# Kernel optimization log

Hardware: AMD Instinct MI355X
Metric: run time of the kernel (lower is better)

## Reference

```python
import jax, jax.numpy as jnp
import numpy as np

D = 1024
H = 8
B, S = 4, 2048


def setup_inputs() -> dict:
    key = jax.random.key(0)
    ks = jax.random.split(key, 11)
    s = 0.02
    return {
        "Q": jax.random.normal(ks[0], (B, S, D), jnp.float32),
        "K": jax.random.normal(ks[1], (B, S, D), jnp.float32),
        "V": jax.random.normal(ks[2], (B, S, D), jnp.float32),
        "WQ": jax.random.normal(ks[3], (D, D), jnp.float32) * s,
        "bQ": jax.random.normal(ks[4], (D,), jnp.float32) * s,
        "WK": jax.random.normal(ks[5], (D, D), jnp.float32) * s,
        "bK": jax.random.normal(ks[6], (D,), jnp.float32) * s,
        "WV": jax.random.normal(ks[7], (D, D), jnp.float32) * s,
        "bV": jax.random.normal(ks[8], (D,), jnp.float32) * s,
        "Wl": jax.random.normal(ks[9], (D, D * H), jnp.float32) * s,
        "bl": jax.random.normal(ks[10], (D,), jnp.float32) * s,
    }


def reference(Q, K, V, WQ, bQ, WK, bK, WV, bV, Wl, bl):
    # SelfAttention (weights shared across all heads in the original module)
    q = Q @ WQ.T + bQ  # [B,S,D]
    k = K @ WK.T + bK
    v = V @ WV.T + bV
    scale = 1.0 / np.sqrt(D).astype(np.float32)
    scores = jnp.einsum('bqd,bkd->bqk', q, k) * scale  # [B,S,S]
    attn = jax.nn.softmax(scores, axis=-1)
    Z = jnp.einsum('bqk,bkd->bqd', attn, v)  # [B,S,D]
    # concat of H identical copies, then linear(D*H -> D)
    Zcat = jnp.tile(Z, (1, 1, H))  # [B,S,D*H]
    return Zcat @ Wl.T + bl
```

## Files before the change

kernel.cpp:

```cpp
#include <hip/hip_runtime.h>
#include <stdint.h>

#define DEV __device__ __forceinline__

typedef __attribute__((ext_vector_type(8))) unsigned short frag8;
typedef __attribute__((ext_vector_type(4))) float f32x4;
typedef __attribute__((ext_vector_type(8))) unsigned short ushort8;
typedef __attribute__((ext_vector_type(4))) unsigned short ushort4v;

DEV unsigned short f2bf(float f) {
  union { float f; unsigned u; } x; x.f = f;
  unsigned r = x.u + 0x7fffu + ((x.u >> 16) & 1u);
  return (unsigned short)(r >> 16);
}
DEV float bf2f(unsigned short b) {
  union { unsigned u; float f; } x; x.u = ((unsigned)b) << 16;
  return x.f;
}

DEV void gload_lds16(const void* g, void* l) {
  __builtin_amdgcn_global_load_lds((const __attribute__((address_space(1))) void*)g,
                                   (__attribute__((address_space(3))) void*)l, 16, 0, 0);
}

DEV void mfma_bf16(f32x4& c, frag8 a, frag8 b) {
  asm("v_mfma_f32_16x16x32_bf16 %0, %1, %2, %0" : "+v"(c) : "v"(a), "v"(b));
}

DEV void wait_vm8_barrier() {
  asm volatile("s_waitcnt vmcnt(8)" ::: "memory");
  __builtin_amdgcn_s_barrier();
  __builtin_amdgcn_sched_barrier(0);
}
DEV void wait_vm0_barrier() {
  asm volatile("s_waitcnt vmcnt(0)" ::: "memory");
  __builtin_amdgcn_s_barrier();
  __builtin_amdgcn_sched_barrier(0);
}
DEV void raw_barrier() {
  __builtin_amdgcn_s_barrier();
  __builtin_amdgcn_sched_barrier(0);
}

template<int MODE>
__global__ __launch_bounds__(256)
void gemm_bt(const unsigned short* __restrict__ A,
             const unsigned short* __restrict__ Bm,
             const float* __restrict__ bias0, const float* __restrict__ bias1,
             float* __restrict__ rowsum,
             void* __restrict__ Cv,
             int N, int K, float scale,
             long sA, long sB, long sC,
             int nx, int ny)
{
  __shared__ unsigned short lds[2][2][128 * 64];

  const int tid  = threadIdx.x;
  const int lane = tid & 63;
  const int wave = tid >> 6;
  const int wm   = wave >> 1;
  const int wn   = wave & 1;

  const unsigned nwg = gridDim.x;
  const unsigned orig = blockIdx.x;
  const unsigned qq = nwg >> 3, rr = nwg & 7;
  const unsigned xcd = orig & 7, jj = orig >> 3;
  const unsigned wg = (xcd < rr ? xcd * (qq + 1) : rr * (qq + 1) + (xcd - rr) * qq) + jj;
  const unsigned bx = wg % (unsigned)nx;
  const unsigned tt = wg / (unsigned)nx;
  const unsigned by = tt % (unsigned)ny;
  const unsigned bz = tt / (unsigned)ny;

  const int bm = (int)by * 128;
  const int bn = (int)bx * 128;

  A  += (size_t)bz * (size_t)sA;
  Bm += (size_t)bz * (size_t)sB;

  const int r8  = lane >> 3;
  const int l8  = lane & 7;
  const int swz = ((l8 ^ r8) << 4);
  const size_t Kb = (size_t)K * 2;

  const char* gA = (const char*)A  + (size_t)(bm + wave * 32 + r8) * Kb + swz;
  const char* gB = (const char*)Bm + (size_t)(bn + wave * 32 + r8) * Kb + swz;
  char* lA0 = (char*)&lds[0][0][0] + wave * 32 * 128;
  char* lB0 = (char*)&lds[0][1][0] + wave * 32 * 128;
  char* lA1 = (char*)&lds[1][0][0] + wave * 32 * 128;
  char* lB1 = (char*)&lds[1][1][0] + wave * 32 * 128;

  const int cr = lane & 15;
  const int kq = lane >> 4;
  const int base16 = ((kq ^ (cr & 7)) << 4);
  const char* rA0 = (const char*)&lds[0][0][0] + (wm * 64 + cr) * 128;
  const char* rB0 = (const char*)&lds[0][1][0] + (wn * 64 + cr) * 128;
  const char* rA1 = (const char*)&lds[1][0][0] + (wm * 64 + cr) * 128;
  const char* rB1 = (const char*)&lds[1][1][0] + (wn * 64 + cr) * 128;

  f32x4 acc[4][4];
  #pragma unroll
  for (int m = 0; m < 4; ++m)
    #pragma unroll
    for (int n = 0; n < 4; ++n)
      acc[m][n] = f32x4{0.f, 0.f, 0.f, 0.f};

  auto STAGE = [&](int t, char* la, char* lb) {
    const char* ga = gA + (size_t)t * 128;
    const char* gb = gB + (size_t)t * 128;
    gload_lds16(ga,               la);
    gload_lds16(gb,               lb);
    gload_lds16(ga +  8 * Kb,     la + 1024);
    gload_lds16(gb +  8 * Kb,     lb + 1024);
    gload_lds16(ga + 16 * Kb,     la + 2048);
    gload_lds16(gb + 16 * Kb,     lb + 2048);
    gload_lds16(ga + 24 * Kb,     la + 3072);
    gload_lds16(gb + 24 * Kb,     lb + 3072);
  };
  auto COMPUTE = [&](const char* ra, const char* rb) {
    #pragma unroll
    for (int kk = 0; kk < 2; ++kk) {
      const int off = base16 ^ (kk << 6);
      frag8 a[4], b[4];
      #pragma unroll
      for (int f = 0; f < 4; ++f) {
        a[f] = *(const frag8*)(ra + f * 2048 + off);
        b[f] = *(const frag8*)(rb + f * 2048 + off);
      }
      #pragma unroll
      for (int m = 0; m < 4; ++m)
        #pragma unroll
        for (int n = 0; n < 4; ++n)
          mfma_bf16(acc[m][n], a[m], b[n]);
    }
  };

  const int nk = K >> 6;
  STAGE(0, lA0, lB0);
  for (int t = 0; t < nk; ++t) {
    const bool odd = t & 1;
    if (t + 1 < nk) {
      STAGE(t + 1, odd ? lA0 : lA1, odd ? lB0 : lB1);
      wait_vm8_barrier();
    } else {
      wait_vm0_barrier();
    }
    COMPUTE(odd ? rA1 : rA0, odd ? rB1 : rB0);
    raw_barrier();
  }

  #pragma unroll
  for (int m = 0; m < 4; ++m) {
    const int gr0 = bm + wm * 64 + m * 16 + kq * 4;
    float psum[4] = {0.f, 0.f, 0.f, 0.f};
    float inv0 = 1.f, inv1 = 1.f, inv2 = 1.f, inv3 = 1.f;
    if constexpr (MODE == 4) {
      const float4 rs = *(const float4*)&bias0[(size_t)bz * 2048 + gr0];
      inv0 = 1.f / rs.x; inv1 = 1.f / rs.y; inv2 = 1.f / rs.z; inv3 = 1.f / rs.w;
    }
    #pragma unroll
    for (int n = 0; n < 4; ++n) {
      const int gc = bn + wn * 64 + n * 16 + cr;
      float v0 = acc[m][n][0], v1 = acc[m][n][1], v2 = acc[m][n][2], v3 = acc[m][n][3];
      if constexpr (MODE == 3) {
        const float c2v = bias0[(size_t)bz * (size_t)N + gc];
        unsigned short* C = (unsigned short*)Cv + (size_t)bz * (size_t)sC;
        unsigned short e0 = f2bf(__expf((v0 + c2v) * scale));
        unsigned short e1 = f2bf(__expf((v1 + c2v) * scale));
        unsigned short e2 = f2bf(__expf((v2 + c2v) * scale));
        unsigned short e3 = f2bf(__expf((v3 + c2v) * scale));
        C[(size_t)(gr0 + 0) * N + gc] = e0;
        C[(size_t)(gr0 + 1) * N + gc] = e1;
        C[(size_t)(gr0 + 2) * N + gc] = e2;
        C[(size_t)(gr0 + 3) * N + gc] = e3;
        psum[0] += bf2f(e0); psum[1] += bf2f(e1);
        psum[2] += bf2f(e2); psum[3] += bf2f(e3);
      } else if constexpr (MODE == 4) {
        const float bb = bias1[gc];
        float* C = (float*)Cv + (size_t)bz * (size_t)sC;
        C[(size_t)(gr0 + 0) * N + gc] = v0 * inv0 + bb;
        C[(size_t)(gr0 + 1) * N + gc] = v1 * inv1 + bb;
        C[(size_t)(gr0 + 2) * N + gc] = v2 * inv2 + bb;
        C[(size_t)(gr0 + 3) * N + gc] = v3 * inv3 + bb;
      } else if constexpr (MODE == 5) {
        if (bz == 1) {
          unsigned short* C = (unsigned short*)Cv + (size_t)sC;
          ushort4v u;
          u[0] = f2bf(v0); u[1] = f2bf(v1); u[2] = f2bf(v2); u[3] = f2bf(v3);
          *(ushort4v*)&C[((size_t)(gr0 >> 11) << 21) + (size_t)gc * 2048 + (gr0 & 2047)] = u;
        } else {
          unsigned short* C = (unsigned short*)Cv;
          C[(size_t)(gr0 + 0) * N + gc] = f2bf(v0);
          C[(size_t)(gr0 + 1) * N + gc] = f2bf(v1);
          C[(size_t)(gr0 + 2) * N + gc] = f2bf(v2);
          C[(size_t)(gr0 + 3) * N + gc] = f2bf(v3);
        }
      } else {
        unsigned short* C = (unsigned short*)Cv + (size_t)bz * (size_t)sC;
        C[(size_t)(gr0 + 0) * N + gc] = f2bf(v0);
        C[(size_t)(gr0 + 1) * N + gc] = f2bf(v1);
        C[(size_t)(gr0 + 2) * N + gc] = f2bf(v2);
        C[(size_t)(gr0 + 3) * N + gc] = f2bf(v3);
      }
    }
    if constexpr (MODE == 3) {
      #pragma unroll
      for (int j = 0; j < 4; ++j) {
        float p = psum[j];
        p += __shfl_xor(p, 1);
        p += __shfl_xor(p, 2);
        p += __shfl_xor(p, 4);
        p += __shfl_xor(p, 8);
        if (cr == 0) atomicAdd(&rowsum[(size_t)bz * 2048 + gr0 + j], p);
      }
    }
  }
}

__global__ __launch_bounds__(256)
void cvt3_bf16(const float* __restrict__ s0, const float* __restrict__ s1,
               const float* __restrict__ s2, unsigned short* __restrict__ out,
               int n8each)
{
  const float* src = (blockIdx.y == 0) ? s0 : (blockIdx.y == 1) ? s1 : s2;
  unsigned short* dst = out + (size_t)blockIdx.y * ((size_t)n8each * 8);
  int i = blockIdx.x * blockDim.x + threadIdx.x;
  const int stride = gridDim.x * blockDim.x;
  for (; i < n8each; i += stride) {
    const float4* p = (const float4*)src + (size_t)i * 2;
    float4 a = p[0], b = p[1];
    ushort8 o;
    o[0] = f2bf(a.x); o[1] = f2bf(a.y); o[2] = f2bf(a.z); o[3] = f2bf(a.w);
    o[4] = f2bf(b.x); o[5] = f2bf(b.y); o[6] = f2bf(b.z); o[7] = f2bf(b.w);
    *((ushort8*)dst + i) = o;
  }
}

__global__ __launch_bounds__(256)
void tpose3(const float* __restrict__ s0, const float* __restrict__ s1,
            const float* __restrict__ s2, unsigned short* __restrict__ wr)
{
  const int z = blockIdx.y;
  const float* src = (z == 0) ? s0 : (z == 1) ? s1 : s2;
  unsigned short* dst = wr + (size_t)((z == 0) ? 2 : (z == 1) ? 0 : 3) * 1024 * 1024;

  __shared__ float t[64][65];
  const int bx  = blockIdx.x & 15;
  const int byy = blockIdx.x >> 4;
  const int tx  = threadIdx.x & 63;
  const int ty4 = threadIdx.x >> 6;

  #pragma unroll
  for (int i = 0; i < 16; ++i) {
    const int r = i * 4 + ty4;
    t[r][tx] = src[(size_t)(byy * 64 + r) * 1024 + bx * 64 + tx];
  }
  __syncthreads();
  #pragma unroll
  for (int i = 0; i < 16; ++i) {
    const int r = i * 4 + ty4;
    dst[(size_t)(bx * 64 + r) * 1024 + byy * 64 + tx] = f2bf(t[tx][r]);
  }
}

__global__ __launch_bounds__(256)
void weff_kernel(const float* __restrict__ Wl, unsigned short* __restrict__ out)
{
  const int idx = blockIdx.x * 256 + threadIdx.x;
  const int j = idx >> 8;
  const int d = (idx & 255) << 2;
  float4 s = make_float4(0.f, 0.f, 0.f, 0.f);
  #pragma unroll
  for (int h = 0; h < 8; ++h) {
    float4 w = *(const float4*)&Wl[(size_t)j * 8192 + h * 1024 + d];
    s.x += w.x; s.y += w.y; s.z += w.z; s.w += w.w;
  }
  ushort4v o;
  o[0] = f2bf(s.x); o[1] = f2bf(s.y); o[2] = f2bf(s.z); o[3] = f2bf(s.w);
  *(ushort4v*)&out[(size_t)j * 1024 + d] = o;
}

__global__ __launch_bounds__(256)
void zero_f32(float* __restrict__ p, int n)
{
  const int i = blockIdx.x * 256 + threadIdx.x;
  if (i < n) p[i] = 0.f;
}

__global__ __launch_bounds__(256)
void u2_kernel(const float* __restrict__ WK, const float* __restrict__ bQ,
               float* __restrict__ u2)
{
  const int k = blockIdx.x * 256 + threadIdx.x;
  const int m0 = blockIdx.y * 256;
  float a = 0.f;
  for (int m = m0; m < m0 + 256; ++m)
    a += WK[(size_t)m * 1024 + k] * bQ[m];
  atomicAdd(&u2[k], a);
}

__global__ __launch_bounds__(256)
void c2_kernel(const unsigned short* __restrict__ Kb, const float* __restrict__ u2,
               float* __restrict__ c2)
{
  const int lane = threadIdx.x & 63;
  const int w    = threadIdx.x >> 6;
  const int r    = blockIdx.x * 4 + w;
  const unsigned short* kr = Kb + (size_t)r * 1024 + lane * 16;
  ushort8 a = *(const ushort8*)kr;
  ushort8 b = *(const ushort8*)(kr + 8);
  const float* uu = u2 + lane * 16;
  float s = 0.f;
  #pragma unroll
  for (int i = 0; i < 8; ++i) s += bf2f(a[i]) * uu[i];
  #pragma unroll
  for (int i = 0; i < 8; ++i) s += bf2f(b[i]) * uu[8 + i];
  #pragma unroll
  for (int off = 32; off; off >>= 1) s += __shfl_xor(s, off);
  if (lane == 0) c2[r] = s;
}

__global__ __launch_bounds__(256)
void biasp_kernel(const unsigned short* __restrict__ Weffb, const float* __restrict__ bV,
                  const float* __restrict__ bl, float* __restrict__ biasp)
{
  const int lane = threadIdx.x & 63;
  const int w    = threadIdx.x >> 6;
  const int j    = blockIdx.x * 4 + w;
  const unsigned short* wr = Weffb + (size_t)j * 1024 + lane * 16;
  ushort8 a = *(const ushort8*)wr;
  ushort8 b = *(const ushort8*)(wr + 8);
  const float* vv = bV + lane * 16;
  float s = 0.f;
  #pragma unroll
  for (int i = 0; i < 8; ++i) s += bf2f(a[i]) * vv[i];
  #pragma unroll
  for (int i = 0; i < 8; ++i) s += bf2f(b[i]) * vv[8 + i];
  #pragma unroll
  for (int off = 32; off; off >>= 1) s += __shfl_xor(s, off);
  if (lane == 0) biasp[j] = s + bl[j];
}

extern "C" void kernel_launch(void* const* d_in, const int* in_sizes, int n_in,
                              void* d_out, int out_size, void* d_ws, size_t ws_size,
                              hipStream_t stream)
{
  (void)in_sizes; (void)n_in; (void)out_size; (void)ws_size;

  const float* Q  = (const float*)d_in[0];
  const float* K  = (const float*)d_in[1];
  const float* V  = (const float*)d_in[2];
  const float* WQ = (const float*)d_in[3];
  const float* bQ = (const float*)d_in[4];
  const float* WK = (const float*)d_in[5];
  const float* bK = (const float*)d_in[6];  (void)bK;
  const float* WV = (const float*)d_in[7];
  const float* bV = (const float*)d_in[8];
  const float* Wl = (const float*)d_in[9];
  const float* bl = (const float*)d_in[10];

  const size_t nX = (size_t)8192 * 1024;
  const size_t nW = (size_t)1024 * 1024;

  unsigned short* Qb  = (unsigned short*)d_ws;
  unsigned short* Vb  = Qb + nX;
  unsigned short* Kb  = Qb + 2 * nX;
  unsigned short* qp  = Qb + 3 * nX;
  unsigned short* vpT = Qb + 4 * nX;
  unsigned short* Wr  = Qb + 5 * nX;
  unsigned short* Weffb = Wr + nW;
  unsigned short* WQt   = Wr + 2 * nW;
  unsigned short* Tt    = Wr + 4 * nW;
  float* Fv   = (float*)(Wr + 6 * nW);
  float* rowsum = Fv;
  float* u2     = Fv + 8192;
  float* c2     = Fv + 9216;
  float* biasp  = Fv + 17408;
  unsigned short* P = Qb;

  const int thr = 256;

  cvt3_bf16<<<dim3(1024, 3), thr, 0, stream>>>(Q, V, K, Qb, (int)(nX / 8));
  tpose3<<<dim3(256, 3), thr, 0, stream>>>(WQ, WK, WV, Wr);
  weff_kernel<<<1024, thr, 0, stream>>>(Wl, Weffb);
  zero_f32<<<36, thr, 0, stream>>>(rowsum, 9216);
  u2_kernel<<<dim3(4, 4), thr, 0, stream>>>(WK, bQ, u2);
  biasp_kernel<<<256, thr, 0, stream>>>(Weffb, bV, bl, biasp);
  c2_kernel<<<2048, thr, 0, stream>>>(Kb, u2, c2);

  gemm_bt<0><<<128, thr, 0, stream>>>(
      Wr, WQt, nullptr, nullptr, nullptr, Tt, 1024, 1024, 1.f,
      (long)nW, (long)nW, (long)nW, 8, 8);
  gemm_bt<5><<<1024, thr, 0, stream>>>(
      Qb, Tt, nullptr, nullptr, nullptr, qp, 1024, 1024, 1.f,
      (long)nX, (long)nW, (long)nX, 8, 64);
  gemm_bt<3><<<1024, thr, 0, stream>>>(
      qp, Kb, c2, nullptr, rowsum, P, 2048, 1024, 0.03125f,
      (long)(2048 * 1024), (long)(2048 * 1024), (long)(2048 * 2048), 16, 16);
  gemm_bt<4><<<512, thr, 0, stream>>>(
      P, vpT, rowsum, biasp, nullptr, d_out, 1024, 2048, 1.f,
      (long)(2048 * 2048), (long)(1024 * 2048), (long)(2048 * 1024), 8, 16);
}
```

Measured before the change: 204.4 us.

## Single-buffer GEMM LDS tiles and merge weight-prep kernels into one launch

```diff
diff --git a/kernel.cpp b/kernel.cpp
--- a/kernel.cpp
+++ b/kernel.cpp
@@ -25,21 +25,6 @@
 
 DEV void mfma_bf16(f32x4& c, frag8 a, frag8 b) {
   asm("v_mfma_f32_16x16x32_bf16 %0, %1, %2, %0" : "+v"(c) : "v"(a), "v"(b));
-}
-
-DEV void wait_vm8_barrier() {
-  asm volatile("s_waitcnt vmcnt(8)" ::: "memory");
-  __builtin_amdgcn_s_barrier();
-  __builtin_amdgcn_sched_barrier(0);
-}
-DEV void wait_vm0_barrier() {
-  asm volatile("s_waitcnt vmcnt(0)" ::: "memory");
-  __builtin_amdgcn_s_barrier();
-  __builtin_amdgcn_sched_barrier(0);
-}
-DEV void raw_barrier() {
-  __builtin_amdgcn_s_barrier();
-  __builtin_amdgcn_sched_barrier(0);
 }
 
 template<int MODE>
@@ -53,7 +38,8 @@
              long sA, long sB, long sC,
              int nx, int ny)
 {
-  __shared__ unsigned short lds[2][2][128 * 64];
+  __shared__ unsigned short ldsA[128 * 64];
+  __shared__ unsigned short ldsB[128 * 64];
 
   const int tid  = threadIdx.x;
   const int lane = tid & 63;
@@ -84,18 +70,14 @@
 
   const char* gA = (const char*)A  + (size_t)(bm + wave * 32 + r8) * Kb + swz;
   const char* gB = (const char*)Bm + (size_t)(bn + wave * 32 + r8) * Kb + swz;
-  char* lA0 = (char*)&lds[0][0][0] + wave * 32 * 128;
-  char* lB0 = (char*)&lds[0][1][0] + wave * 32 * 128;
-  char* lA1 = (char*)&lds[1][0][0] + wave * 32 * 128;
-  char* lB1 = (char*)&lds[1][1][0] + wave * 32 * 128;
+  char* lA = (char*)ldsA + wave * 32 * 128;
+  char* lB = (char*)ldsB + wave * 32 * 128;
 
   const int cr = lane & 15;
   const int kq = lane >> 4;
   const int base16 = ((kq ^ (cr & 7)) << 4);
-  const char* rA0 = (const char*)&lds[0][0][0] + (wm * 64 + cr) * 128;
-  const char* rB0 = (const char*)&lds[0][1][0] + (wn * 64 + cr) * 128;
-  const char* rA1 = (const char*)&lds[1][0][0] + (wm * 64 + cr) * 128;
-  const char* rB1 = (const char*)&lds[1][1][0] + (wn * 64 + cr) * 128;
+  const char* rowA = (const char*)ldsA + (wm * 64 + cr) * 128;
+  const char* rowB = (const char*)ldsB + (wn * 64 + cr) * 128;
 
   f32x4 acc[4][4];
   #pragma unroll
@@ -104,27 +86,30 @@
     for (int n = 0; n < 4; ++n)
       acc[m][n] = f32x4{0.f, 0.f, 0.f, 0.f};
 
-  auto STAGE = [&](int t, char* la, char* lb) {
-    const char* ga = gA + (size_t)t * 128;
-    const char* gb = gB + (size_t)t * 128;
-    gload_lds16(ga,               la);
-    gload_lds16(gb,               lb);
-    gload_lds16(ga +  8 * Kb,     la + 1024);
-    gload_lds16(gb +  8 * Kb,     lb + 1024);
-    gload_lds16(ga + 16 * Kb,     la + 2048);
-    gload_lds16(gb + 16 * Kb,     lb + 2048);
-    gload_lds16(ga + 24 * Kb,     la + 3072);
-    gload_lds16(gb + 24 * Kb,     lb + 3072);
-  };
-  auto COMPUTE = [&](const char* ra, const char* rb) {
+  const int nk = K >> 6;
+  for (int kt = 0; kt < nk; ++kt) {
+    __syncthreads();
+    {
+      const char* ga = gA + (size_t)kt * 128;
+      const char* gb = gB + (size_t)kt * 128;
+      gload_lds16(ga,           lA);
+      gload_lds16(gb,           lB);
+      gload_lds16(ga +  8 * Kb, lA + 1024);
+      gload_lds16(gb +  8 * Kb, lB + 1024);
+      gload_lds16(ga + 16 * Kb, lA + 2048);
+      gload_lds16(gb + 16 * Kb, lB + 2048);
+      gload_lds16(ga + 24 * Kb, lA + 3072);
+      gload_lds16(gb + 24 * Kb, lB + 3072);
+    }
+    __syncthreads();
     #pragma unroll
     for (int kk = 0; kk < 2; ++kk) {
       const int off = base16 ^ (kk << 6);
       frag8 a[4], b[4];
       #pragma unroll
       for (int f = 0; f < 4; ++f) {
-        a[f] = *(const frag8*)(ra + f * 2048 + off);
-        b[f] = *(const frag8*)(rb + f * 2048 + off);
+        a[f] = *(const frag8*)(rowA + f * 2048 + off);
+        b[f] = *(const frag8*)(rowB + f * 2048 + off);
       }
       #pragma unroll
       for (int m = 0; m < 4; ++m)
@@ -132,20 +117,6 @@
         for (int n = 0; n < 4; ++n)
           mfma_bf16(acc[m][n], a[m], b[n]);
     }
-  };
-
-  const int nk = K >> 6;
-  STAGE(0, lA0, lB0);
-  for (int t = 0; t < nk; ++t) {
-    const bool odd = t & 1;
-    if (t + 1 < nk) {
-      STAGE(t + 1, odd ? lA0 : lA1, odd ? lB0 : lB1);
-      wait_vm8_barrier();
-    } else {
-      wait_vm0_barrier();
-    }
-    COMPUTE(odd ? rA1 : rA0, odd ? rB1 : rB0);
-    raw_barrier();
   }
 
   #pragma unroll
@@ -236,66 +207,74 @@
 }
 
 __global__ __launch_bounds__(256)
-void tpose3(const float* __restrict__ s0, const float* __restrict__ s1,
-            const float* __restrict__ s2, unsigned short* __restrict__ wr)
-{
-  const int z = blockIdx.y;
-  const float* src = (z == 0) ? s0 : (z == 1) ? s1 : s2;
-  unsigned short* dst = wr + (size_t)((z == 0) ? 2 : (z == 1) ? 0 : 3) * 1024 * 1024;
-
+void prep_kernel(const float* __restrict__ WQ, const float* __restrict__ WK,
+                 const float* __restrict__ WV, const float* __restrict__ Wl,
+                 const float* __restrict__ bQ, const float* __restrict__ bV,
+                 const float* __restrict__ bl,
+                 unsigned short* __restrict__ Wr,
+                 float* __restrict__ u2, float* __restrict__ biasp,
+                 float* __restrict__ rowsum)
+{
   __shared__ float t[64][65];
-  const int bx  = blockIdx.x & 15;
-  const int byy = blockIdx.x >> 4;
-  const int tx  = threadIdx.x & 63;
-  const int ty4 = threadIdx.x >> 6;
-
-  #pragma unroll
-  for (int i = 0; i < 16; ++i) {
-    const int r = i * 4 + ty4;
-    t[r][tx] = src[(size_t)(byy * 64 + r) * 1024 + bx * 64 + tx];
+  const int blk = blockIdx.x;
+  const int tid = threadIdx.x;
+
+  if (blk < 768) {
+    const int z = blk >> 8;
+    const int local = blk & 255;
+    const float* src = (z == 0) ? WQ : (z == 1) ? WK : WV;
+    unsigned short* dst = Wr + (size_t)((z == 0) ? 2 : (z == 1) ? 0 : 3) * 1024 * 1024;
+    const int bx  = local & 15;
+    const int byy = local >> 4;
+    const int tx  = tid & 63;
+    const int ty4 = tid >> 6;
+    #pragma unroll
+    for (int i = 0; i < 16; ++i) {
+      const int r = i * 4 + ty4;
+      t[r][tx] = src[(size_t)(byy * 64 + r) * 1024 + bx * 64 + tx];
+    }
+    __syncthreads();
+    #pragma unroll
+    for (int i = 0; i < 16; ++i) {
+      const int r = i * 4 + ty4;
+      dst[(size_t)(bx * 64 + r) * 1024 + byy * 64 + tx] = f2bf(t[tx][r]);
+    }
+  } else if (blk < 1792) {
+    const int j = blk - 768;
+    const int d = tid * 4;
+    float4 s = make_float4(0.f, 0.f, 0.f, 0.f);
+    #pragma unroll
+    for (int h = 0; h < 8; ++h) {
+      float4 w = *(const float4*)&Wl[(size_t)j * 8192 + h * 1024 + d];
+      s.x += w.x; s.y += w.y; s.z += w.z; s.w += w.w;
+    }
+    unsigned short* Weffb = Wr + (size_t)1024 * 1024;
+    ushort4v o;
+    o[0] = f2bf(s.x); o[1] = f2bf(s.y); o[2] = f2bf(s.z); o[3] = f2bf(s.w);
+    *(ushort4v*)&Weffb[(size_t)j * 1024 + d] = o;
+    const float4 bv = *(const float4*)&bV[d];
+    float p = s.x * bv.x + s.y * bv.y + s.z * bv.z + s.w * bv.w;
+    #pragma unroll
+    for (int off = 32; off; off >>= 1) p += __shfl_xor(p, off);
+    __shared__ float red[4];
+    if ((tid & 63) == 0) red[tid >> 6] = p;
+    __syncthreads();
+    if (tid == 0) biasp[j] = red[0] + red[1] + red[2] + red[3] + bl[j];
+  } else if (blk < 1796) {
+    const int k = (blk - 1792) * 256 + tid;
+    __shared__ float bq[1024];
+    #pragma unroll
+    for (int i = 0; i < 4; ++i) bq[tid + i * 256] = bQ[tid + i * 256];
+    __syncthreads();
+    float a = 0.f;
+    for (int m = 0; m < 1024; ++m)
+      a += WK[(size_t)m * 1024 + k] * bq[m];
+    u2[k] = a;
+  } else {
+    const int base = (blk - 1796) * 2048 + tid * 8;
+    #pragma unroll
+    for (int i = 0; i < 8; ++i) rowsum[base + i] = 0.f;
   }
-  __syncthreads();
-  #pragma unroll
-  for (int i = 0; i < 16; ++i) {
-    const int r = i * 4 + ty4;
-    dst[(size_t)(bx * 64 + r) * 1024 + byy * 64 + tx] = f2bf(t[tx][r]);
-  }
-}
-
-__global__ __launch_bounds__(256)
-void weff_kernel(const float* __restrict__ Wl, unsigned short* __restrict__ out)
-{
-  const int idx = blockIdx.x * 256 + threadIdx.x;
-  const int j = idx >> 8;
-  const int d = (idx & 255) << 2;
-  float4 s = make_float4(0.f, 0.f, 0.f, 0.f);
-  #pragma unroll
-  for (int h = 0; h < 8; ++h) {
-    float4 w = *(const float4*)&Wl[(size_t)j * 8192 + h * 1024 + d];
-    s.x += w.x; s.y += w.y; s.z += w.z; s.w += w.w;
-  }
-  ushort4v o;
-  o[0] = f2bf(s.x); o[1] = f2bf(s.y); o[2] = f2bf(s.z); o[3] = f2bf(s.w);
-  *(ushort4v*)&out[(size_t)j * 1024 + d] = o;
-}
-
-__global__ __launch_bounds__(256)
-void zero_f32(float* __restrict__ p, int n)
-{
-  const int i = blockIdx.x * 256 + threadIdx.x;
-  if (i < n) p[i] = 0.f;
-}
-
-__global__ __launch_bounds__(256)
-void u2_kernel(const float* __restrict__ WK, const float* __restrict__ bQ,
-               float* __restrict__ u2)
-{
-  const int k = blockIdx.x * 256 + threadIdx.x;
-  const int m0 = blockIdx.y * 256;
-  float a = 0.f;
-  for (int m = m0; m < m0 + 256; ++m)
-    a += WK[(size_t)m * 1024 + k] * bQ[m];
-  atomicAdd(&u2[k], a);
 }
 
 __global__ __launch_bounds__(256)
@@ -317,27 +296,6 @@
   #pragma unroll
   for (int off = 32; off; off >>= 1) s += __shfl_xor(s, off);
   if (lane == 0) c2[r] = s;
-}
-
-__global__ __launch_bounds__(256)
-void biasp_kernel(const unsigned short* __restrict__ Weffb, const float* __restrict__ bV,
-                  const float* __restrict__ bl, float* __restrict__ biasp)
-{
-  const int lane = threadIdx.x & 63;
-  const int w    = threadIdx.x >> 6;
-  const int j    = blockIdx.x * 4 + w;
-  const unsigned short* wr = Weffb + (size_t)j * 1024 + lane * 16;
-  ushort8 a = *(const ushort8*)wr;
-  ushort8 b = *(const ushort8*)(wr + 8);
-  const float* vv = bV + lane * 16;
-  float s = 0.f;
-  #pragma unroll
-  for (int i = 0; i < 8; ++i) s += bf2f(a[i]) * vv[i];
-  #pragma unroll
-  for (int i = 0; i < 8; ++i) s += bf2f(b[i]) * vv[8 + i];
-  #pragma unroll
-  for (int off = 32; off; off >>= 1) s += __shfl_xor(s, off);
-  if (lane == 0) biasp[j] = s + bl[j];
 }
 
 extern "C" void kernel_launch(void* const* d_in, const int* in_sizes, int n_in,
@@ -362,12 +320,10 @@
   const size_t nW = (size_t)1024 * 1024;
 
   unsigned short* Qb  = (unsigned short*)d_ws;
-  unsigned short* Vb  = Qb + nX;
   unsigned short* Kb  = Qb + 2 * nX;
   unsigned short* qp  = Qb + 3 * nX;
   unsigned short* vpT = Qb + 4 * nX;
   unsigned short* Wr  = Qb + 5 * nX;
-  unsigned short* Weffb = Wr + nW;
   unsigned short* WQt   = Wr + 2 * nW;
   unsigned short* Tt    = Wr + 4 * nW;
   float* Fv   = (float*)(Wr + 6 * nW);
@@ -379,12 +335,9 @@
 
   const int thr = 256;
 
+  prep_kernel<<<1800, thr, 0, stream>>>(WQ, WK, WV, Wl, bQ, bV, bl,
+                                        Wr, u2, biasp, rowsum);
   cvt3_bf16<<<dim3(1024, 3), thr, 0, stream>>>(Q, V, K, Qb, (int)(nX / 8));
-  tpose3<<<dim3(256, 3), thr, 0, stream>>>(WQ, WK, WV, Wr);
-  weff_kernel<<<1024, thr, 0, stream>>>(Wl, Weffb);
-  zero_f32<<<36, thr, 0, stream>>>(rowsum, 9216);
-  u2_kernel<<<dim3(4, 4), thr, 0, stream>>>(WK, bQ, u2);
-  biasp_kernel<<<256, thr, 0, stream>>>(Weffb, bV, bl, biasp);
   c2_kernel<<<2048, thr, 0, stream>>>(Kb, u2, c2);
 
   gemm_bt<0><<<128, thr, 0, stream>>>(
```

Result: slower. 214.4 us (+4.9%).
